# Kernel tuning notes

Measured on AMD Instinct MI355X. Metric: run time of the kernel, lower is better.

## Reference

```python
import jax, jax.numpy as jnp
import numpy as np

W = 8            # fine window (sqrt of feat_0's WW)
WP2 = W + 2      # feat_1 search window side (10)
SLICE = 8
TEMP = 10.0


def setup_inputs() -> dict:
    key = jax.random.key(0)
    ks = jax.random.split(key, 6)
    M = 8192
    C = 64
    return {
        'feat_0': jax.random.normal(ks[0], (M, W * W, C), dtype=jnp.float32),
        'feat_1': jax.random.normal(ks[1], (M, WP2 * WP2, C), dtype=jnp.float32),
        'mkpts0_c': jax.random.uniform(ks[2], (M, 2), dtype=jnp.float32) * 800.0,
        'mkpts1_c': jax.random.uniform(ks[3], (M, 2), dtype=jnp.float32) * 800.0,
        'mconf': jax.random.uniform(ks[4], (M,), dtype=jnp.float32),
        'b_ids': jnp.zeros((M,), dtype=jnp.int64),
        'hw0_i': 832,
        'hw0_f': 416,
        'bs': 1,
    }


def reference(feat_0, feat_1, mkpts0_c, mkpts1_c, mconf, b_ids, hw0_i, hw0_f, bs):
    M, WW, C = feat_0.shape                      # WW = W*W = 64
    scale = float(hw0_i) / float(hw0_f)          # image -> fine-feature stride

    feat_f0, feat_ff0 = feat_0[..., :-SLICE], feat_0[..., -SLICE:]
    feat_f1, feat_ff1 = feat_1[..., :-SLICE], feat_1[..., -SLICE:]

    # note: BOTH sides divided by sqrt(C) in the source -> overall 1/C
    conf_f = jnp.einsum('mlc,mrc->mlr', feat_f0, feat_f1) * (1.0 / C)          # [M,64,100]
    conf_ff = jnp.einsum('mlc,mrc->mlr', feat_ff0, feat_ff1) / np.sqrt(SLICE)  # [M,64,100]

    # dual softmax, then crop the 10x10 search window to the inner 8x8
    sm = jax.nn.softmax(conf_f, axis=1) * jax.nn.softmax(conf_f, axis=2)
    sm = sm.reshape(M, WW, WP2, WP2)[..., 1:-1, 1:-1].reshape(M, WW, WW)       # [M,64,64]

    # ---- get_fine_ds_match (torch.no_grad in source) ----
    flat = jax.lax.stop_gradient(sm.reshape(M, WW * WW))
    idx = jnp.argmax(flat, axis=-1)                # [M]
    idx_l, idx_r = idx // WW, idx % WW             # each in [0,64)
    gy, gx = jnp.meshgrid(jnp.arange(W), jnp.arange(W), indexing='ij')
    grid = (jnp.stack([gx, gy], -1).reshape(WW, 2).astype(feat_0.dtype)
            - (W // 2) + 0.5)                      # (x,y) pixel offsets, centered
    delta_l = grid[idx_l]                          # [M,2]
    delta_r = grid[idx_r]
    mkpts0_f = jax.lax.stop_gradient(mkpts0_c) + delta_l * scale
    mkpts1_mid = jax.lax.stop_gradient(mkpts1_c) + delta_r * scale

    # ---- 3x3 window gather in the (W+2)x(W+2) map (faithful index arithmetic) ----
    iids, jids = idx_r // W, idx_r % W             # [0,8)
    d = jnp.arange(3) - 1                          # {-1,0,1}
    wi = iids[:, None, None] + d[None, :, None]    # [M,3,3] rows, may be -1
    wj = jids[:, None, None] + d[None, None, :]    # [M,3,3] cols
    wi = jnp.where(wi < 0, wi + WP2, wi)           # torch negative-index wrap
    wj = jnp.where(wj < 0, wj + WP2, wj)
    cff = conf_ff.reshape(M, WW, WP2, WP2)
    win = cff[jnp.arange(M)[:, None, None], idx_l[:, None, None], wi, wj]  # [M,3,3]

    probs = jax.nn.softmax(win.reshape(M, 9) / TEMP, axis=-1)              # [M,9]
    heat = probs.reshape(M, 3, 3)
    pos = jnp.linspace(-1.0, 1.0, 3).astype(feat_0.dtype)
    coord_x = jnp.sum(heat * pos[None, None, :], axis=(1, 2))              # over width
    coord_y = jnp.sum(heat * pos[None, :, None], axis=(1, 2))              # over height
    coords = jnp.stack([coord_x, coord_y], -1)     # [M,2] soft-argmax, (x,y)

    scale1 = scale                                 # bs == 1 branch
    mkpts1_f = mkpts1_mid + coords * (3 // 2) * scale1
    return (mkpts0_f, mkpts1_f, probs, sm)
```

## Files before the change

### kernel.cpp

```cpp
#include <hip/hip_runtime.h>
#include <math.h>
#include <limits.h>


constexpr int TPB = 256;

typedef _Float16 half8_t __attribute__((ext_vector_type(8)));
typedef _Float16 half4_t __attribute__((ext_vector_type(4)));
typedef float    float4_t __attribute__((ext_vector_type(4)));

struct __align__(16) SMem {
    union {
        struct {
            unsigned short f1h[100 * 56];
            unsigned short f1l[100 * 56];
        };
        float sm[64 * 64];
    };
    float cpart[4][112];
    float csum[112];
    float wval[4];
    int   widx[4];
    float win[9];
};

__global__ __launch_bounds__(TPB, 6) void fine_matching_kernel(
    const float* __restrict__ feat0,
    const float* __restrict__ feat1,
    const float* __restrict__ mk0,
    const float* __restrict__ mk1,
    const int* __restrict__ hw0_i,
    const int* __restrict__ hw0_f,
    float* __restrict__ out, int M)
{
    __shared__ SMem S;

    const int m = blockIdx.x;
    const int t = threadIdx.x;
    const int lane = t & 63;
    const int w = t >> 6;
    const int col = lane & 15;
    const int q = lane >> 4;
    const float scale = (float)hw0_i[0] / (float)hw0_f[0];

    const float* g0 = feat0 + (size_t)m * 4096;
    const float* g1 = feat1 + (size_t)m * 6400;
    _Float16* f1h = (_Float16*)S.f1h;
    _Float16* f1l = (_Float16*)S.f1l;

    const int arow = (16 * w + col) * 64;
    float4_t araw[2][2];
    #pragma unroll
    for (int ks = 0; ks < 2; ks++) {
        const int koff = ks ? (32 + q * 8) : (q * 8);
        araw[ks][0] = *(const float4_t*)(g0 + arow + koff);
        araw[ks][1] = *(const float4_t*)(g0 + arow + koff + 4);
    }

    for (int i = t; i < 1600; i += TPB) {
        const int fl = i << 2, l = fl >> 6, c = fl & 63;
        if (c >= 56) continue;
        float4_t v = ((const float4_t*)g1)[i];
        half4_t hi, lo;
        #pragma unroll
        for (int j = 0; j < 4; j++) {
            float x = v[j];
            _Float16 h = (_Float16)x;
            hi[j] = h;
            lo[j] = (_Float16)(x - (float)h);
        }
        *(half4_t*)(f1h + l * 56 + c) = hi;
        *(half4_t*)(f1l + l * 56 + c) = lo;
    }

    half8_t hz;
    #pragma unroll
    for (int j = 0; j < 8; j++) hz[j] = (_Float16)0.0f;

    half8_t ah[2], al[2];
    #pragma unroll
    for (int ks = 0; ks < 2; ks++) {
        #pragma unroll
        for (int j = 0; j < 8; j++) {
            float x = araw[ks][j >> 2][j & 3];
            _Float16 h = (_Float16)x;
            ah[ks][j] = h;
            al[ks][j] = (_Float16)(x - (float)h);
        }
    }
    if (q == 3) { ah[1] = hz; al[1] = hz; }

    __syncthreads();

    float4_t acc[7];
    #pragma unroll
    for (int rt = 0; rt < 7; rt++)
        #pragma unroll
        for (int j = 0; j < 4; j++) acc[rt][j] = 0.0f;

    #pragma unroll
    for (int ks = 0; ks < 2; ks++) {
        const int koff = ks ? (32 + q * 8) : (q * 8);
        const bool kz = (ks == 1) && (q == 3);
        const int bkoff = kz ? 0 : koff;
        #pragma unroll
        for (int rt = 0; rt < 7; rt++) {
            int brow = rt * 16 + col;
            if (brow > 99) brow = 99;
            const int bo = brow * 56 + bkoff;
            half8_t bh = *(const half8_t*)(f1h + bo);
            half8_t bl = *(const half8_t*)(f1l + bo);
            acc[rt] = __builtin_amdgcn_mfma_f32_16x16x32_f16(ah[ks], bh, acc[rt], 0, 0, 0);
            acc[rt] = __builtin_amdgcn_mfma_f32_16x16x32_f16(al[ks], bh, acc[rt], 0, 0, 0);
            acc[rt] = __builtin_amdgcn_mfma_f32_16x16x32_f16(ah[ks], bl, acc[rt], 0, 0, 0);
        }
    }

    float p[7][4];
    #pragma unroll
    for (int rt = 0; rt < 7; rt++) {
        const bool rvalid = (rt < 6) || (col < 4);
        #pragma unroll
        for (int j = 0; j < 4; j++) {
            float c = acc[rt][j] * (1.0f / 64.0f);
            p[rt][j] = rvalid ? __expf(c) : 0.0f;
        }
    }

    float invr[4];
    #pragma unroll
    for (int j = 0; j < 4; j++) {
        float s = 0.0f;
        #pragma unroll
        for (int rt = 0; rt < 7; rt++) s += p[rt][j];
        s += __shfl_xor(s, 1); s += __shfl_xor(s, 2);
        s += __shfl_xor(s, 4); s += __shfl_xor(s, 8);
        invr[j] = 1.0f / s;
    }

    #pragma unroll
    for (int rt = 0; rt < 7; rt++) {
        float s = p[rt][0] + p[rt][1] + p[rt][2] + p[rt][3];
        s += __shfl_xor(s, 16);
        s += __shfl_xor(s, 32);
        if (lane < 16) S.cpart[w][rt * 16 + col] = s;
    }
    __syncthreads();
    if (t < 112)
        S.csum[t] = S.cpart[0][t] + S.cpart[1][t] + S.cpart[2][t] + S.cpart[3][t];
    __syncthreads();

    float invc[7];
    #pragma unroll
    for (int rt = 0; rt < 7; rt++) {
        const bool rvalid = (rt < 6) || (col < 4);
        invc[rt] = rvalid ? 1.0f / S.csum[rt * 16 + col] : 0.0f;
    }

    float* s_sm = S.sm;
    float bestv = -INFINITY; int besti = INT_MAX;
    #pragma unroll
    for (int j = 0; j < 4; j++) {
        const int l = 16 * w + 4 * q + j;
        #pragma unroll
        for (int rt = 0; rt < 7; rt++) {
            const int r = rt * 16 + col;
            if (r < 100) {
                const int ri = r / 10, rj = r - ri * 10;
                if (ri >= 1 && ri <= 8 && rj >= 1 && rj <= 8) {
                    float pv = p[rt][j];
                    float v = pv * pv * invr[j] * invc[rt];
                    int flat = l * 64 + (ri - 1) * 8 + (rj - 1);
                    s_sm[flat] = v;
                    if (v > bestv) { bestv = v; besti = flat; }
                }
            }
        }
    }
    #pragma unroll
    for (int d = 1; d < 64; d <<= 1) {
        float ov = __shfl_xor(bestv, d);
        int   oi = __shfl_xor(besti, d);
        if (ov > bestv || (ov == bestv && oi < besti)) { bestv = ov; besti = oi; }
    }
    if (lane == 0) { S.wval[w] = bestv; S.widx[w] = besti; }
    __syncthreads();

    float bv = S.wval[0]; int best = S.widx[0];
    #pragma unroll
    for (int i = 1; i < 4; i++) {
        float v2 = S.wval[i]; int i2 = S.widx[i];
        if (v2 > bv || (v2 == bv && i2 < best)) { bv = v2; best = i2; }
    }
    const int idx_l = best >> 6;
    const int idx_r = best & 63;
    const int iids  = idx_r >> 3, jids = idx_r & 7;

    float* o_sm = out + (size_t)13 * M + (size_t)m * 4096;
    for (int i = t; i < 1024; i += TPB)
        ((float4_t*)o_sm)[i] = ((const float4_t*)s_sm)[i];

    if (t < 9) {
        int da = t / 3 - 1, db = t % 3 - 1;
        int wi = iids + da; if (wi < 0) wi += 10;
        int wj = jids + db; if (wj < 0) wj += 10;
        int rp = wi * 10 + wj;
        float4_t a0 = *(const float4_t*)(g0 + idx_l * 64 + 56);
        float4_t a1 = *(const float4_t*)(g0 + idx_l * 64 + 60);
        float4_t b0 = *(const float4_t*)(g1 + rp * 64 + 56);
        float4_t b1 = *(const float4_t*)(g1 + rp * 64 + 60);
        float dot = 0.0f;
        #pragma unroll
        for (int j = 0; j < 4; j++) dot += a0[j] * b0[j] + a1[j] * b1[j];
        S.win[t] = dot * 0.35355339059327373f;
    }
    __syncthreads();

    if (t == 0) {
        float ww[9], mx = -INFINITY;
        #pragma unroll
        for (int i = 0; i < 9; i++) { ww[i] = S.win[i] * 0.1f; mx = fmaxf(mx, ww[i]); }
        float sum = 0.0f;
        #pragma unroll
        for (int i = 0; i < 9; i++) { ww[i] = __expf(ww[i] - mx); sum += ww[i]; }
        float inv = 1.0f / sum;
        float* o_probs = out + (size_t)4 * M + (size_t)m * 9;
        float cx = 0.0f, cy = 0.0f;
        #pragma unroll
        for (int i = 0; i < 9; i++) {
            float pb = ww[i] * inv;
            o_probs[i] = pb;
            cx += pb * (float)(i % 3 - 1);
            cy += pb * (float)(i / 3 - 1);
        }
        float dlx = (float)(idx_l & 7) - 3.5f;
        float dly = (float)(idx_l >> 3) - 3.5f;
        out[2 * m]     = mk0[2 * m]     + dlx * scale;
        out[2 * m + 1] = mk0[2 * m + 1] + dly * scale;
        float drx = (float)jids - 3.5f;
        float dry = (float)iids - 3.5f;
        float* o1 = out + (size_t)2 * M;
        o1[2 * m]     = mk1[2 * m]     + (drx + cx) * scale;
        o1[2 * m + 1] = mk1[2 * m + 1] + (dry + cy) * scale;
    }
}

extern "C" void kernel_launch(void* const* d_in, const int* in_sizes, int n_in,
                              void* d_out, int out_size, void* d_ws, size_t ws_size,
                              hipStream_t stream) {
    const float* feat0 = (const float*)d_in[0];
    const float* feat1 = (const float*)d_in[1];
    const float* mk0   = (const float*)d_in[2];
    const float* mk1   = (const float*)d_in[3];
    const int*   hw0_i = (const int*)d_in[6];
    const int*   hw0_f = (const int*)d_in[7];
    const int M = in_sizes[0] / 4096;

    fine_matching_kernel<<<M, TPB, 0, stream>>>(
        feat0, feat1, mk0, mk1, hw0_i, hw0_f, (float*)d_out, M);
}
```

Measured before the change: 421.8 us.

## Overlay reduction scratch onto f1 staging buffer and raise occupancy target

Moves the column-sum, argmax and window scratch arrays into the union with the fp16 feat_1 staging buffer, shrinking shared memory per block. A barrier after the MFMA loop keeps the overlay safe. Launch bounds go from 6 to 7 blocks per SM. The feat_1 staging loop now does 700 iterations of 8-wide loads and half8 stores in place of 1600 with skipped lanes. The gain from higher occupancy must outweigh the extra barrier and possible register pressure from the tighter launch bound.

Result: no change. 418.8 us (-0.7%).

```diff
diff --git a/kernel.cpp b/kernel.cpp
--- a/kernel.cpp
+++ b/kernel.cpp
@@ -15,16 +15,18 @@
             unsigned short f1h[100 * 56];
             unsigned short f1l[100 * 56];
         };
-        float sm[64 * 64];
+        struct {
+            float sm[64 * 64];
+            float cpart[4][112];
+            float csum[112];
+            float wval[4];
+            int   widx[4];
+            float win[9];
+        };
     };
-    float cpart[4][112];
-    float csum[112];
-    float wval[4];
-    int   widx[4];
-    float win[9];
 };
 
-__global__ __launch_bounds__(TPB, 6) void fine_matching_kernel(
+__global__ __launch_bounds__(TPB, 7) void fine_matching_kernel(
     const float* __restrict__ feat0,
     const float* __restrict__ feat1,
     const float* __restrict__ mk0,
@@ -57,20 +59,29 @@
         araw[ks][1] = *(const float4_t*)(g0 + arow + koff + 4);
     }
 
-    for (int i = t; i < 1600; i += TPB) {
-        const int fl = i << 2, l = fl >> 6, c = fl & 63;
-        if (c >= 56) continue;
-        float4_t v = ((const float4_t*)g1)[i];
-        half4_t hi, lo;
-        #pragma unroll
-        for (int j = 0; j < 4; j++) {
-            float x = v[j];
+    for (int i = t; i < 700; i += TPB) {
+        const int l = i / 7;
+        const int c = (i - l * 7) * 8;
+        const float* src = g1 + l * 64 + c;
+        float4_t v0 = *(const float4_t*)(src);
+        float4_t v1 = *(const float4_t*)(src + 4);
+        half8_t hi, lo;
+        #pragma unroll
+        for (int k = 0; k < 4; k++) {
+            float x = v0[k];
             _Float16 h = (_Float16)x;
-            hi[j] = h;
-            lo[j] = (_Float16)(x - (float)h);
-        }
-        *(half4_t*)(f1h + l * 56 + c) = hi;
-        *(half4_t*)(f1l + l * 56 + c) = lo;
+            hi[k] = h;
+            lo[k] = (_Float16)(x - (float)h);
+        }
+        #pragma unroll
+        for (int k = 0; k < 4; k++) {
+            float x = v1[k];
+            _Float16 h = (_Float16)x;
+            hi[4 + k] = h;
+            lo[4 + k] = (_Float16)(x - (float)h);
+        }
+        *(half8_t*)(f1h + l * 56 + c) = hi;
+        *(half8_t*)(f1l + l * 56 + c) = lo;
     }
 
     half8_t hz;
@@ -115,6 +126,8 @@
             acc[rt] = __builtin_amdgcn_mfma_f32_16x16x32_f16(ah[ks], bl, acc[rt], 0, 0, 0);
         }
     }
+
+    __syncthreads();
 
     float p[7][4];
     #pragma unroll
```
